# Optimization experiments

Hardware: AMD Instinct MI355X
Metric: run time of the kernel (lower is better)

## Reference

```python
import jax, jax.numpy as jnp
import numpy as np
import math

B, S, D, H, CD = 8, 1024, 1024, 16, 512
HD = D // H
LN_EPS = 1e-5


def _layernorm(x, g, b):
    mu = jnp.mean(x, axis=-1, keepdims=True)
    var = jnp.var(x, axis=-1, keepdims=True)
    return (x - mu) / jnp.sqrt(var + LN_EPS) * g + b


def _modlin(x, code, wc_w, wc_b, ln_g, ln_b, W, b):
    # transformed_code: LayerNorm(Linear(code)) -> [D]
    tc = _layernorm(code @ wc_w.T + wc_b, ln_g, ln_b)
    return (tc * x) @ W.T + b


def setup_inputs() -> dict:
    key = jax.random.key(0)
    ks = jax.random.split(key, 16)
    inp = {
        'query': jax.random.normal(ks[0], (B, S, D), jnp.float32),
        'key': jax.random.normal(ks[1], (B, S, D), jnp.float32),
        'value': jax.random.normal(ks[2], (B, S, D), jnp.float32),
        'compability_u': jax.random.uniform(ks[3], (B, S), jnp.float32),
        'code': jax.random.normal(ks[4], (CD,), jnp.float32),
        'W': jax.random.normal(ks[5], (D, D), jnp.float32) * 0.02,
        'b': jnp.zeros((D,), jnp.float32),
    }
    for i, p in enumerate(['q', 'k', 'v', 'o']):
        inp[p + '_wc_w'] = jax.random.normal(ks[6 + i], (D, CD), jnp.float32) * 0.02
        inp[p + '_wc_b'] = jnp.zeros((D,), jnp.float32)
        inp[p + '_ln_g'] = jnp.ones((D,), jnp.float32)
        inp[p + '_ln_b'] = jnp.zeros((D,), jnp.float32)
    return inp


def reference(query, key, value, compability_u, code, W, b,
              q_wc_w, q_wc_b, q_ln_g, q_ln_b,
              k_wc_w, k_wc_b, k_ln_g, k_ln_b,
              v_wc_w, v_wc_b, v_ln_g, v_ln_b,
              o_wc_w, o_wc_b, o_ln_g, o_ln_b):
    Q = _modlin(query, code, q_wc_w, q_wc_b, q_ln_g, q_ln_b, W, b)
    K = _modlin(key, code, k_wc_w, k_wc_b, k_ln_g, k_ln_b, W, b)
    V = _modlin(value, code, v_wc_w, v_wc_b, v_ln_g, v_ln_b, W, b)
    # [B,S,D] -> [B,H,S,HD]
    Q = Q.reshape(B, S, H, HD).transpose(0, 2, 1, 3)
    K = K.reshape(B, S, H, HD).transpose(0, 2, 1, 3)
    V = V.reshape(B, S, H, HD).transpose(0, 2, 1, 3)
    energy = jnp.einsum('bhid,bhjd->bhij', Q, K) / math.sqrt(HD)
    attention = jax.nn.softmax(energy, axis=-1)
    # c_u_i[b,h,i,j] = u[b,i]; c_u_j[b,h,i,j] = u[b,j]
    attention = compability_u[:, None, :, None] * compability_u[:, None, None, :] * attention
    attention = attention / (1e-6 + attention)
    x = jnp.einsum('bhij,bhjd->bhid', attention, V)  # dropout p=0 (eval)
    x = x.transpose(0, 2, 1, 3).reshape(B, S, D)
    x = _modlin(x, code, o_wc_w, o_wc_b, o_ln_g, o_ln_b, W, b)
    return x, attention
```

## Files before the change

### kernel.cpp

```cpp
#include <hip/hip_runtime.h>
#include <hip/hip_bf16.h>
#include <stdint.h>

typedef __bf16 bf16_t;
typedef __attribute__((ext_vector_type(8))) __bf16 bf16x8;
typedef __attribute__((ext_vector_type(4))) float f32x4;

#define B_  8
#define S_  1024
#define D_  1024
#define H_  16
#define HD_ 64
#define CD_ 512

typedef __attribute__((address_space(1))) const unsigned int* gas_ptr;
typedef __attribute__((address_space(3))) unsigned int* las_ptr;

__device__ __forceinline__ void gl2lds16(const void* g, void* l) {
    __builtin_amdgcn_global_load_lds((gas_ptr)(unsigned long long)g,
                                     (las_ptr)(unsigned long long)l, 16, 0, 0);
}

__device__ __forceinline__ float clamp30(float x) {
    return fminf(fmaxf(x, -30.f), 30.f);
}

__global__ void detect_kernel(const unsigned int* Wbits, int* flag) {
    __shared__ int cnt[64];
    int c = 0;
    for (int i = threadIdx.x; i < 512; i += 64) {
        unsigned int w = Wbits[i];
        unsigned int e = (w >> 7) & 0xFFu;
        c += (e >= 0x66u && e <= 0x7Fu) ? 1 : 0;
    }
    cnt[threadIdx.x] = c;
    __syncthreads();
    if (threadIdx.x == 0) {
        int t = 0;
        for (int i = 0; i < 64; ++i) t += cnt[i];
        *flag = (t >= 280) ? 0 : 1;
    }
}

#define CANON_TOTAL 28333568u
struct CanonArgs {
    const void* src[23];
    bf16_t* dst[23];
    unsigned int off[24];
    const int* flag;
};

__global__ __launch_bounds__(256) void canon_kernel(CanonArgs a) {
    const bool f32 = (*a.flag != 0);
    const unsigned int e = ((unsigned int)blockIdx.x * 256u + threadIdx.x) * 8u;
    if (e >= CANON_TOTAL) return;
    int t = 0;
    while (e >= a.off[t + 1]) ++t;
    const unsigned int le = e - a.off[t];
    bf16_t* d = a.dst[t] + le;
    if (f32) {
        const float* s = (const float*)a.src[t] + le;
        bf16x8 o;
#pragma unroll
        for (int j = 0; j < 8; ++j) o[j] = (bf16_t)s[j];
        *(bf16x8*)d = o;
    } else {
        *(uint4*)d = *(const uint4*)((const bf16_t*)a.src[t] + le);
    }
}

struct TCArgs {
    const bf16_t* code;
    const bf16_t* bglob;
    const bf16_t* wcw[4];
    const bf16_t* wcb[4];
    const bf16_t* lng[4];
    const bf16_t* lnb[4];
    float* tc;
    float* biasArr;
};

__global__ __launch_bounds__(256) void tc_kernel(TCArgs a) {
    const int p = blockIdx.x;
    const int tid = threadIdx.x;
    __shared__ float codeS[CD_];
    __shared__ float red[256];
    __shared__ float bcast[2];
    for (int c = tid; c < CD_; c += 256) codeS[c] = (float)a.code[c];
    __syncthreads();
    float y[4];
    const bf16_t* wcw = a.wcw[p];
    for (int j = 0; j < 4; ++j) {
        const int d = tid + j * 256;
        float acc = (float)a.wcb[p][d];
        const bf16x8* row = (const bf16x8*)(wcw + (size_t)d * CD_);
        for (int c8 = 0; c8 < CD_ / 8; ++c8) {
            bf16x8 v = row[c8];
#pragma unroll
            for (int t = 0; t < 8; ++t) acc += codeS[c8 * 8 + t] * (float)v[t];
        }
        y[j] = acc;
    }
    float s = y[0] + y[1] + y[2] + y[3];
    red[tid] = s;
    __syncthreads();
    for (int off = 128; off > 0; off >>= 1) {
        if (tid < off) red[tid] += red[tid + off];
        __syncthreads();
    }
    if (tid == 0) bcast[0] = red[0] * (1.0f / (float)D_);
    __syncthreads();
    const float mu = bcast[0];
    float sq = 0.f;
    for (int j = 0; j < 4; ++j) { float t = y[j] - mu; sq += t * t; }
    red[tid] = sq;
    __syncthreads();
    for (int off = 128; off > 0; off >>= 1) {
        if (tid < off) red[tid] += red[tid + off];
        __syncthreads();
    }
    if (tid == 0) bcast[1] = red[0] * (1.0f / (float)D_);
    __syncthreads();
    const float rstd = rsqrtf(bcast[1] + 1e-5f);
    const float scale = (p == 0) ? 0.125f : 1.0f;
    for (int j = 0; j < 4; ++j) {
        const int d = tid + j * 256;
        float tcv = ((y[j] - mu) * rstd * (float)a.lng[p][d] + (float)a.lnb[p][d]) * scale;
        a.tc[p * D_ + d] = tcv;
        a.biasArr[p * D_ + d] = (float)a.bglob[d] * scale;
    }
}

__global__ __launch_bounds__(256) void wscale_kernel(const bf16_t* __restrict__ W,
                                                     const float* __restrict__ tc,
                                                     bf16_t* __restrict__ Wp) {
    const size_t idx = (size_t)blockIdx.x * 256 + threadIdx.x;
    const size_t e = idx * 8;
    const int p = (int)(e >> 20);
    const size_t rem = e & 1048575;
    const int k = (int)(rem & 1023);
    bf16x8 w = *(const bf16x8*)(W + rem);
    const float* t = tc + p * 1024 + k;
    bf16x8 o;
#pragma unroll
    for (int j = 0; j < 8; ++j) o[j] = (bf16_t)((float)w[j] * t[j]);
    *(bf16x8*)(Wp + e) = o;
}

__global__ __launch_bounds__(256) void gemm_bt(const bf16_t* __restrict__ A0,
                                               const bf16_t* __restrict__ A1,
                                               const bf16_t* __restrict__ A2,
                                               const bf16_t* __restrict__ WpAll,
                                               const float* __restrict__ biasAll,
                                               void* Cbase, int pBase, int dualOut,
                                               const int* flagp) {
    constexpr int Kd = 1024, Nd = 1024;
    __shared__ __align__(16) bf16_t As[128 * 32];
    __shared__ __align__(16) bf16_t Bs[128 * 32];
    const int tid = threadIdx.x;
    const int bid0 = blockIdx.x + 8 * blockIdx.y;
    const int bids = (bid0 & 7) * gridDim.y + (bid0 >> 3);
    const int bgx = bids & 7, bgy = bids >> 3;
    const int pl = bgy >> 6;
    const int p = pBase + pl;
    const bf16_t* A = (pl == 0) ? A0 : ((pl == 1) ? A1 : A2);
    const bf16_t* Bw = WpAll + (size_t)p * 1024 * 1024;
    const size_t cOff = (size_t)pl * 8388608;
    const int rowBase = (bgy & 63) * 128;
    const int colBase = bgx * 128;
    const int lane = tid & 63;
    const int wv = tid >> 6;
    const int wm = wv >> 1, wn = wv & 1;
    const int qd = lane >> 4, cl = lane & 15;

    f32x4 acc[4][4];
#pragma unroll
    for (int tn = 0; tn < 4; ++tn) {
        float bv = biasAll[p * 1024 + colBase + wn * 64 + tn * 16 + cl];
#pragma unroll
        for (int tm = 0; tm < 4; ++tm) acc[tm][tn] = (f32x4){bv, bv, bv, bv};
    }

    for (int kb = 0; kb < Kd; kb += 32) {
#pragma unroll
        for (int cc = 0; cc < 2; ++cc) {
            const int s = tid + cc * 256;
            const int rw = s >> 2;
            const int co = (s & 3) * 8;
            gl2lds16(A + (size_t)(rowBase + rw) * Kd + kb + co,
                     (char*)As + wv * 1024 + cc * 4096);
            gl2lds16(Bw + (size_t)(colBase + rw) * Kd + kb + co,
                     (char*)Bs + wv * 1024 + cc * 4096);
        }
        __syncthreads();
        bf16x8 aF[4], bF[4];
#pragma unroll
        for (int tm = 0; tm < 4; ++tm)
            aF[tm] = *(const bf16x8*)&As[(wm * 64 + tm * 16 + cl) * 32 + qd * 8];
#pragma unroll
        for (int tn = 0; tn < 4; ++tn)
            bF[tn] = *(const bf16x8*)&Bs[(wn * 64 + tn * 16 + cl) * 32 + qd * 8];
        __builtin_amdgcn_s_setprio(1);
#pragma unroll
        for (int tm = 0; tm < 4; ++tm)
#pragma unroll
            for (int tn = 0; tn < 4; ++tn)
                acc[tm][tn] = __builtin_amdgcn_mfma_f32_16x16x32_bf16(aF[tm], bF[tn],
                                                                      acc[tm][tn], 0, 0, 0);
        __builtin_amdgcn_s_setprio(0);
        __syncthreads();
    }
    const bool f32o = (dualOut != 0) && (*flagp != 0);
    if (f32o) {
        float* Cf = (float*)Cbase + cOff;
#pragma unroll
        for (int tm = 0; tm < 4; ++tm)
#pragma unroll
            for (int tn = 0; tn < 4; ++tn)
#pragma unroll
                for (int r = 0; r < 4; ++r) {
                    const int row = rowBase + wm * 64 + tm * 16 + qd * 4 + r;
                    const int col = colBase + wn * 64 + tn * 16 + cl;
                    Cf[(size_t)row * Nd + col] = acc[tm][tn][r];
                }
    } else {
        bf16_t* Cb = (bf16_t*)Cbase + cOff;
#pragma unroll
        for (int tm = 0; tm < 4; ++tm)
#pragma unroll
            for (int tn = 0; tn < 4; ++tn)
#pragma unroll
                for (int r = 0; r < 4; ++r) {
                    const int row = rowBase + wm * 64 + tm * 16 + qd * 4 + r;
                    const int col = colBase + wn * 64 + tn * 16 + cl;
                    Cb[(size_t)row * Nd + col] = (bf16_t)acc[tm][tn][r];
                }
    }
}

__global__ __launch_bounds__(256) void vtrans(const bf16_t* __restrict__ V,
                                              bf16_t* __restrict__ Vt) {
    __shared__ __align__(16) bf16_t T[64][72];
    const int bh = blockIdx.y, b = bh >> 4, h = bh & 15;
    const int s0 = blockIdx.x * 64;
    const int tid = threadIdx.x;
    const int rr = tid >> 3, cc8 = (tid & 7) * 8;
#pragma unroll
    for (int it = 0; it < 2; ++it) {
        const int sr = rr + it * 32;
        bf16x8 v = *(const bf16x8*)&V[((size_t)(b * S_ + s0 + sr)) * D_ + h * HD_ + cc8];
#pragma unroll
        for (int j = 0; j < 8; ++j) T[cc8 + j][sr] = v[j];
    }
    __syncthreads();
#pragma unroll
    for (int it = 0; it < 2; ++it) {
        const int dr = rr + it * 32;
        bf16x8 o;
#pragma unroll
        for (int j = 0; j < 8; ++j) o[j] = T[dr][cc8 + j];
        *(bf16x8*)&Vt[((size_t)bh * 64 + dr) * S_ + s0 + cc8] = o;
    }
}

__global__ __launch_bounds__(256) void attn_fused(const bf16_t* __restrict__ Q,
                                                  const bf16_t* __restrict__ Kmat,
                                                  const bf16_t* __restrict__ Vt,
                                                  const bf16_t* __restrict__ u,
                                                  void* outBase,
                                                  bf16_t* __restrict__ Xatt,
                                                  const int* flagp) {
    __shared__ __align__(16) bf16_t Ks[2][32 * 64];
    __shared__ __align__(16) bf16_t Vs[2][64 * 32];
    __shared__ __align__(16) bf16_t P[4][512];
    __shared__ __align__(16) bf16_t uS[S_];
    const int bid0 = blockIdx.x + 16 * blockIdx.y;
    const int bids = (bid0 & 7) * 256 + (bid0 >> 3);
    const int bx = bids & 15, bh = bids >> 4;
    const int b = bh >> 4, h = bh & 15;
    const int tid = threadIdx.x, lane = tid & 63, wv = tid >> 6;
    const int i0 = bx * 64 + wv * 16;
    const int qd = lane >> 4, cl = lane & 15;
    const bool f32o = (*flagp != 0);
    float* attF = (float*)outBase + 8388608;
    bf16_t* attB = (bf16_t*)outBase + 8388608;

    for (int t = tid; t < S_ / 8; t += 256)
        *(bf16x8*)&uS[t * 8] = *(const bf16x8*)&u[b * S_ + t * 8];

    const bf16_t* Qb = Q + ((size_t)(b * S_ + i0 + cl)) * D_ + h * HD_ + qd * 8;
    bf16x8 aQ0 = *(const bf16x8*)Qb;
    bf16x8 aQ1 = *(const bf16x8*)(Qb + 32);

    const int srow_k = tid >> 3;
    const int scol_k = ((tid & 7) * 16) ^ ((srow_k & 7) << 4);
    const bf16_t* Ksrc = Kmat + ((size_t)(b * S_) + srow_k) * D_ + h * HD_ + (scol_k >> 1);
    const int srow_v = tid >> 2;
    const int scol_v = ((tid & 3) * 16) ^ ((srow_v & 3) << 4);
    const bf16_t* Vsrc = Vt + ((size_t)bh * 64 + srow_v) * S_ + (scol_v >> 1);

    gl2lds16(Ksrc, (char*)Ks[0] + tid * 16);
    __syncthreads();
    f32x4 l = {0.f, 0.f, 0.f, 0.f};
    for (int jb = 0; jb < S_; jb += 32) {
        const int cur = (jb >> 5) & 1;
        if (jb + 32 < S_)
            gl2lds16(Ksrc + (size_t)(jb + 32) * D_, (char*)Ks[cur ^ 1] + tid * 16);
#pragma unroll
        for (int js = 0; js < 2; ++js) {
            const int rj = js * 16 + cl;
            const char* kr = (const char*)Ks[cur] + rj * 128;
            const int sw = (rj & 7) << 4;
            bf16x8 k0 = *(const bf16x8*)(kr + ((qd * 16) ^ sw));
            bf16x8 k1 = *(const bf16x8*)(kr + ((64 + qd * 16) ^ sw));
            f32x4 e = {0.f, 0.f, 0.f, 0.f};
            __builtin_amdgcn_s_setprio(1);
            e = __builtin_amdgcn_mfma_f32_16x16x32_bf16(aQ0, k0, e, 0, 0, 0);
            e = __builtin_amdgcn_mfma_f32_16x16x32_bf16(aQ1, k1, e, 0, 0, 0);
            __builtin_amdgcn_s_setprio(0);
            l.x += __expf(clamp30(e.x));
            l.y += __expf(clamp30(e.y));
            l.z += __expf(clamp30(e.z));
            l.w += __expf(clamp30(e.w));
        }
        __syncthreads();
    }
    for (int m = 1; m < 16; m <<= 1) {
        l.x += __shfl_xor(l.x, m);
        l.y += __shfl_xor(l.y, m);
        l.z += __shfl_xor(l.z, m);
        l.w += __shfl_xor(l.w, m);
    }
    float ui[4], el[4];
    const float lv[4] = {l.x, l.y, l.z, l.w};
#pragma unroll
    for (int r = 0; r < 4; ++r) {
        ui[r] = (float)uS[i0 + qd * 4 + r];
        el[r] = fmaxf(1e-6f * lv[r], 0.f);
    }

    f32x4 accPV[4];
#pragma unroll
    for (int dt = 0; dt < 4; ++dt) accPV[dt] = (f32x4){0.f, 0.f, 0.f, 0.f};
    bf16_t* Pw = P[wv];

    gl2lds16(Ksrc, (char*)Ks[0] + tid * 16);
    gl2lds16(Vsrc, (char*)Vs[0] + tid * 16);
    __syncthreads();
    for (int jb = 0; jb < S_; jb += 32) {
        const int cur = (jb >> 5) & 1;
        if (jb + 32 < S_) {
            gl2lds16(Ksrc + (size_t)(jb + 32) * D_, (char*)Ks[cur ^ 1] + tid * 16);
            gl2lds16(Vsrc + (jb + 32), (char*)Vs[cur ^ 1] + tid * 16);
        }
#pragma unroll
        for (int js = 0; js < 2; ++js) {
            const int rj = js * 16 + cl;
            const char* kr = (const char*)Ks[cur] + rj * 128;
            const int sw = (rj & 7) << 4;
            bf16x8 k0 = *(const bf16x8*)(kr + ((qd * 16) ^ sw));
            bf16x8 k1 = *(const bf16x8*)(kr + ((64 + qd * 16) ^ sw));
            f32x4 e = {0.f, 0.f, 0.f, 0.f};
            __builtin_amdgcn_s_setprio(1);
            e = __builtin_amdgcn_mfma_f32_16x16x32_bf16(aQ0, k0, e, 0, 0, 0);
            e = __builtin_amdgcn_mfma_f32_16x16x32_bf16(aQ1, k1, e, 0, 0, 0);
            __builtin_amdgcn_s_setprio(0);
            const int j0 = jb + js * 16;
            const float uj = (float)uS[j0 + cl];
#pragma unroll
            for (int r = 0; r < 4; ++r) {
                float t = __expf(clamp30(e[r]));
                float num = ui[r] * uj * t;
                float att = num * __builtin_amdgcn_rcpf(el[r] + num);
                const size_t aidx = ((size_t)bh * S_ + i0 + qd * 4 + r) * S_ + j0 + cl;
                if (f32o) attF[aidx] = att;
                else attB[aidx] = (bf16_t)att;
                Pw[(qd * 4 + r) * 32 + js * 16 + cl] = (bf16_t)att;
            }
        }
        bf16x8 pA = *(const bf16x8*)&Pw[cl * 32 + qd * 8];
        __builtin_amdgcn_s_setprio(1);
#pragma unroll
        for (int dt = 0; dt < 4; ++dt) {
            const int rd = dt * 16 + cl;
            const char* vr = (const char*)Vs[cur] + rd * 64;
            bf16x8 vF = *(const bf16x8*)(vr + ((qd * 16) ^ ((rd & 3) << 4)));
            accPV[dt] = __builtin_amdgcn_mfma_f32_16x16x32_bf16(pA, vF, accPV[dt], 0, 0, 0);
        }
        __builtin_amdgcn_s_setprio(0);
        __syncthreads();
    }
#pragma unroll
    for (int dt = 0; dt < 4; ++dt)
#pragma unroll
        for (int r = 0; r < 4; ++r)
            Xatt[((size_t)(b * S_ + i0 + qd * 4 + r)) * D_ + h * HD_ + dt * 16 + cl] =
                (bf16_t)accPV[dt][r];
}

extern "C" void kernel_launch(void* const* d_in, const int* in_sizes, int n_in,
                              void* d_out, int out_size, void* d_ws, size_t ws_size,
                              hipStream_t stream) {
    float* tc      = (float*)d_ws;
    float* biasArr = tc + 4096;
    bf16_t* Wp     = (bf16_t*)(biasArr + 4096);
    bf16_t* QKV    = Wp + (size_t)4 * 1048576;
    bf16_t* Xatt   = QKV + (size_t)3 * 8388608;
    bf16_t* Vt     = Xatt + 8388608;
    float* lsum    = (float*)(Vt + 8388608);
    bf16_t* smallC = (bf16_t*)(lsum + 131072);
    bf16_t* cu     = smallC;
    bf16_t* ccode  = cu + 8192;
    bf16_t* cb     = ccode + 512;
    bf16_t* cwcb   = cb + 1024;
    bf16_t* clng   = cwcb + 4096;
    bf16_t* clnb   = clng + 4096;
    int* flagp     = (int*)(clnb + 4096);

    char* canonBase = (char*)d_out + 227540992;
    bf16_t* cQ   = (bf16_t*)canonBase;
    bf16_t* cK   = cQ + 8388608;
    bf16_t* cV   = cK + 8388608;
    bf16_t* cW   = cV + 8388608;
    bf16_t* cwcw = cW + 1048576;

    detect_kernel<<<1, 64, 0, stream>>>((const unsigned int*)d_in[5], flagp);

    CanonArgs ca;
    const unsigned int offs[24] = {
        0u, 8388608u, 16777216u, 25165824u, 25174016u, 25174528u, 26223104u, 26224128u,
        26748416u, 26749440u, 26750464u, 26751488u,
        27275776u, 27276800u, 27277824u, 27278848u,
        27803136u, 27804160u, 27805184u, 27806208u,
        28330496u, 28331520u, 28332544u, 28333568u};
    for (int i = 0; i < 24; ++i) ca.off[i] = offs[i];
    ca.flag = flagp;
    ca.src[0] = d_in[0]; ca.dst[0] = cQ;
    ca.src[1] = d_in[1]; ca.dst[1] = cK;
    ca.src[2] = d_in[2]; ca.dst[2] = cV;
    ca.src[3] = d_in[3]; ca.dst[3] = cu;
    ca.src[4] = d_in[4]; ca.dst[4] = ccode;
    ca.src[5] = d_in[5]; ca.dst[5] = cW;
    ca.src[6] = d_in[6]; ca.dst[6] = cb;
    for (int p = 0; p < 4; ++p) {
        ca.src[7 + 4 * p]  = d_in[7 + 4 * p];  ca.dst[7 + 4 * p]  = cwcw + p * 524288;
        ca.src[8 + 4 * p]  = d_in[8 + 4 * p];  ca.dst[8 + 4 * p]  = cwcb + p * 1024;
        ca.src[9 + 4 * p]  = d_in[9 + 4 * p];  ca.dst[9 + 4 * p]  = clng + p * 1024;
        ca.src[10 + 4 * p] = d_in[10 + 4 * p]; ca.dst[10 + 4 * p] = clnb + p * 1024;
    }
    canon_kernel<<<13835, 256, 0, stream>>>(ca);

    TCArgs ta;
    ta.code = ccode;
    ta.bglob = cb;
    for (int p = 0; p < 4; ++p) {
        ta.wcw[p] = cwcw + p * 524288;
        ta.wcb[p] = cwcb + p * 1024;
        ta.lng[p] = clng + p * 1024;
        ta.lnb[p] = clnb + p * 1024;
    }
    ta.tc = tc;
    ta.biasArr = biasArr;
    tc_kernel<<<4, 256, 0, stream>>>(ta);

    wscale_kernel<<<2048, 256, 0, stream>>>(cW, tc, Wp);
    gemm_bt<<<dim3(8, 192), 256, 0, stream>>>(cQ, cK, cV, Wp, biasArr, QKV, 0, 0, flagp);
    vtrans<<<dim3(16, 128), 256, 0, stream>>>(QKV + (size_t)2 * 8388608, Vt);
    attn_fused<<<dim3(16, 128), 256, 0, stream>>>(QKV, QKV + 8388608, Vt, cu, d_out,
                                                  Xatt, flagp);
    gemm_bt<<<dim3(8, 64), 256, 0, stream>>>(Xatt, Xatt, Xatt, Wp, biasArr, d_out, 3, 1,
                                             flagp);
}
```

Measured before the change: 1.006 ms.

## Double-buffer GEMM LDS tiles, fold format detection into canon, widen tc_kernel

The bf16 GEMM now uses two LDS buffers per operand. The global-to-LDS loads for the next K slice are issued before the MFMAs of the current slice, so memory traffic overlaps compute and one barrier per iteration is removed. The separate detect_kernel launch is dropped: every canon_kernel block recomputes the fp32/bf16 format flag from W using a wave shuffle reduction, and block 0 writes it out for later kernels. tc_kernel moves from 256 to 512 threads per block so each thread computes fewer rows. The cost is double the GEMM LDS footprint, which may lower occupancy, plus a small redundant read of W in every canon block.

```diff
diff --git a/kernel.cpp b/kernel.cpp
--- a/kernel.cpp
+++ b/kernel.cpp
@@ -25,34 +25,33 @@
     return fminf(fmaxf(x, -30.f), 30.f);
 }
 
-__global__ void detect_kernel(const unsigned int* Wbits, int* flag) {
-    __shared__ int cnt[64];
-    int c = 0;
-    for (int i = threadIdx.x; i < 512; i += 64) {
-        unsigned int w = Wbits[i];
-        unsigned int e = (w >> 7) & 0xFFu;
-        c += (e >= 0x66u && e <= 0x7Fu) ? 1 : 0;
-    }
-    cnt[threadIdx.x] = c;
-    __syncthreads();
-    if (threadIdx.x == 0) {
-        int t = 0;
-        for (int i = 0; i < 64; ++i) t += cnt[i];
-        *flag = (t >= 280) ? 0 : 1;
-    }
-}
-
 #define CANON_TOTAL 28333568u
 struct CanonArgs {
     const void* src[23];
     bf16_t* dst[23];
     unsigned int off[24];
-    const int* flag;
+    int* flagOut;
 };
 
 __global__ __launch_bounds__(256) void canon_kernel(CanonArgs a) {
-    const bool f32 = (*a.flag != 0);
-    const unsigned int e = ((unsigned int)blockIdx.x * 256u + threadIdx.x) * 8u;
+    __shared__ int flagS;
+    const int tid = threadIdx.x;
+    if (tid < 64) {
+        int c = 0;
+        const unsigned int* wb = (const unsigned int*)a.src[5];
+        for (int i = tid; i < 512; i += 64) {
+            unsigned int w = wb[i];
+            unsigned int ex = (w >> 7) & 0xFFu;
+            c += (ex >= 0x66u && ex <= 0x7Fu) ? 1 : 0;
+        }
+        for (int m = 1; m < 64; m <<= 1) c += __shfl_xor(c, m);
+        if (tid == 0) flagS = (c >= 280) ? 0 : 1;
+    }
+    __syncthreads();
+    const bool f32 = (flagS != 0);
+    if (blockIdx.x == 0 && tid == 0) *a.flagOut = flagS;
+
+    const unsigned int e = ((unsigned int)blockIdx.x * 256u + tid) * 8u;
     if (e >= CANON_TOTAL) return;
     int t = 0;
     while (e >= a.off[t + 1]) ++t;
@@ -80,18 +79,18 @@
     float* biasArr;
 };
 
-__global__ __launch_bounds__(256) void tc_kernel(TCArgs a) {
+__global__ __launch_bounds__(512) void tc_kernel(TCArgs a) {
     const int p = blockIdx.x;
     const int tid = threadIdx.x;
     __shared__ float codeS[CD_];
-    __shared__ float red[256];
+    __shared__ float red[512];
     __shared__ float bcast[2];
-    for (int c = tid; c < CD_; c += 256) codeS[c] = (float)a.code[c];
-    __syncthreads();
-    float y[4];
+    for (int c = tid; c < CD_; c += 512) codeS[c] = (float)a.code[c];
+    __syncthreads();
+    float y[2];
     const bf16_t* wcw = a.wcw[p];
-    for (int j = 0; j < 4; ++j) {
-        const int d = tid + j * 256;
+    for (int j = 0; j < 2; ++j) {
+        const int d = tid + j * 512;
         float acc = (float)a.wcb[p][d];
         const bf16x8* row = (const bf16x8*)(wcw + (size_t)d * CD_);
         for (int c8 = 0; c8 < CD_ / 8; ++c8) {
@@ -101,10 +100,9 @@
         }
         y[j] = acc;
     }
-    float s = y[0] + y[1] + y[2] + y[3];
-    red[tid] = s;
-    __syncthreads();
-    for (int off = 128; off > 0; off >>= 1) {
+    red[tid] = y[0] + y[1];
+    __syncthreads();
+    for (int off = 256; off > 0; off >>= 1) {
         if (tid < off) red[tid] += red[tid + off];
         __syncthreads();
     }
@@ -112,10 +110,10 @@
     __syncthreads();
     const float mu = bcast[0];
     float sq = 0.f;
-    for (int j = 0; j < 4; ++j) { float t = y[j] - mu; sq += t * t; }
+    for (int j = 0; j < 2; ++j) { float t = y[j] - mu; sq += t * t; }
     red[tid] = sq;
     __syncthreads();
-    for (int off = 128; off > 0; off >>= 1) {
+    for (int off = 256; off > 0; off >>= 1) {
         if (tid < off) red[tid] += red[tid + off];
         __syncthreads();
     }
@@ -123,8 +121,8 @@
     __syncthreads();
     const float rstd = rsqrtf(bcast[1] + 1e-5f);
     const float scale = (p == 0) ? 0.125f : 1.0f;
-    for (int j = 0; j < 4; ++j) {
-        const int d = tid + j * 256;
+    for (int j = 0; j < 2; ++j) {
+        const int d = tid + j * 512;
         float tcv = ((y[j] - mu) * rstd * (float)a.lng[p][d] + (float)a.lnb[p][d]) * scale;
         a.tc[p * D_ + d] = tcv;
         a.biasArr[p * D_ + d] = (float)a.bglob[d] * scale;
@@ -155,8 +153,8 @@
                                                void* Cbase, int pBase, int dualOut,
                                                const int* flagp) {
     constexpr int Kd = 1024, Nd = 1024;
-    __shared__ __align__(16) bf16_t As[128 * 32];
-    __shared__ __align__(16) bf16_t Bs[128 * 32];
+    __shared__ __align__(16) bf16_t As[2][128 * 32];
+    __shared__ __align__(16) bf16_t Bs[2][128 * 32];
     const int tid = threadIdx.x;
     const int bid0 = blockIdx.x + 8 * blockIdx.y;
     const int bids = (bid0 & 7) * gridDim.y + (bid0 >> 3);
@@ -173,6 +171,14 @@
     const int wm = wv >> 1, wn = wv & 1;
     const int qd = lane >> 4, cl = lane & 15;
 
+    const int rw0 = tid >> 2, rw1 = (tid + 256) >> 2;
+    const int co0 = (tid & 3) * 8, co1 = ((tid + 256) & 3) * 8;
+    const bf16_t* Asrc0 = A + (size_t)(rowBase + rw0) * Kd + co0;
+    const bf16_t* Asrc1 = A + (size_t)(rowBase + rw1) * Kd + co1;
+    const bf16_t* Bsrc0 = Bw + (size_t)(colBase + rw0) * Kd + co0;
+    const bf16_t* Bsrc1 = Bw + (size_t)(colBase + rw1) * Kd + co1;
+    const int ldst0 = wv * 1024 + (tid & 63) * 16;
+
     f32x4 acc[4][4];
 #pragma unroll
     for (int tn = 0; tn < 4; ++tn) {
@@ -180,26 +186,32 @@
 #pragma unroll
         for (int tm = 0; tm < 4; ++tm) acc[tm][tn] = (f32x4){bv, bv, bv, bv};
     }
+    (void)ldst0;
+
+    {
+        gl2lds16(Asrc0, (char*)As[0] + (size_t)tid * 16);
+        gl2lds16(Asrc1, (char*)As[0] + (size_t)(tid + 256) * 16);
+        gl2lds16(Bsrc0, (char*)Bs[0] + (size_t)tid * 16);
+        gl2lds16(Bsrc1, (char*)Bs[0] + (size_t)(tid + 256) * 16);
+    }
+    __syncthreads();
 
     for (int kb = 0; kb < Kd; kb += 32) {
-#pragma unroll
-        for (int cc = 0; cc < 2; ++cc) {
-            const int s = tid + cc * 256;
-            const int rw = s >> 2;
-            const int co = (s & 3) * 8;
-            gl2lds16(A + (size_t)(rowBase + rw) * Kd + kb + co,
-                     (char*)As + wv * 1024 + cc * 4096);
-            gl2lds16(Bw + (size_t)(colBase + rw) * Kd + kb + co,
-                     (char*)Bs + wv * 1024 + cc * 4096);
-        }
-        __syncthreads();
+        const int cur = (kb >> 5) & 1;
+        if (kb + 32 < Kd) {
+            const int nk = kb + 32;
+            gl2lds16(Asrc0 + nk, (char*)As[cur ^ 1] + (size_t)tid * 16);
+            gl2lds16(Asrc1 + nk, (char*)As[cur ^ 1] + (size_t)(tid + 256) * 16);
+            gl2lds16(Bsrc0 + nk, (char*)Bs[cur ^ 1] + (size_t)tid * 16);
+            gl2lds16(Bsrc1 + nk, (char*)Bs[cur ^ 1] + (size_t)(tid + 256) * 16);
+        }
         bf16x8 aF[4], bF[4];
 #pragma unroll
         for (int tm = 0; tm < 4; ++tm)
-            aF[tm] = *(const bf16x8*)&As[(wm * 64 + tm * 16 + cl) * 32 + qd * 8];
+            aF[tm] = *(const bf16x8*)&As[cur][(wm * 64 + tm * 16 + cl) * 32 + qd * 8];
 #pragma unroll
         for (int tn = 0; tn < 4; ++tn)
-            bF[tn] = *(const bf16x8*)&Bs[(wn * 64 + tn * 16 + cl) * 32 + qd * 8];
+            bF[tn] = *(const bf16x8*)&Bs[cur][(wn * 64 + tn * 16 + cl) * 32 + qd * 8];
         __builtin_amdgcn_s_setprio(1);
 #pragma unroll
         for (int tm = 0; tm < 4; ++tm)
@@ -424,8 +436,6 @@
     bf16_t* cW   = cV + 8388608;
     bf16_t* cwcw = cW + 1048576;
 
-    detect_kernel<<<1, 64, 0, stream>>>((const unsigned int*)d_in[5], flagp);
-
     CanonArgs ca;
     const unsigned int offs[24] = {
         0u, 8388608u, 16777216u, 25165824u, 25174016u, 25174528u, 26223104u, 26224128u,
@@ -434,7 +444,7 @@
         27803136u, 27804160u, 27805184u, 27806208u,
         28330496u, 28331520u, 28332544u, 28333568u};
     for (int i = 0; i < 24; ++i) ca.off[i] = offs[i];
-    ca.flag = flagp;
+    ca.flagOut = flagp;
     ca.src[0] = d_in[0]; ca.dst[0] = cQ;
     ca.src[1] = d_in[1]; ca.dst[1] = cK;
     ca.src[2] = d_in[2]; ca.dst[2] = cV;
@@ -461,7 +471,7 @@
     }
     ta.tc = tc;
     ta.biasArr = biasArr;
-    tc_kernel<<<4, 256, 0, stream>>>(ta);
+    tc_kernel<<<4, 512, 0, stream>>>(ta);
 
     wscale_kernel<<<2048, 256, 0, stream>>>(cW, tc, Wp);
     gemm_bt<<<dim3(8, 192), 256, 0, stream>>>(cQ, cK, cV, Wp, biasArr, QKV, 0, 0, flagp);
```

Result: faster. 946.0 us (-6.0%).
